# Performance work log

Measured on AMD Instinct MI355X. Metric: run time of the kernel, lower is better.

## Reference

```python
import jax, jax.numpy as jnp
import numpy as np

B, D = 2048, 1024
TEMP = 0.1
LAMBDA_CS_REG = 0.5


def setup_inputs() -> dict:
    key = jax.random.key(0)
    k1, k2, k3, k4, k5 = jax.random.split(key, 5)
    return {
        "english": jax.random.normal(k1, (B, D), dtype=jnp.float32),
        "etok": jax.random.normal(k2, (B, D), dtype=jnp.float32),
        "ktoe": jax.random.normal(k3, (B, D), dtype=jnp.float32),
        "korean": jax.random.normal(k4, (B, D), dtype=jnp.float32),
        "cs_ratios": jax.random.uniform(k5, (B,), dtype=jnp.float32),
    }


def _l2norm(x):
    return x / jnp.linalg.norm(x, axis=1, keepdims=True)


def reference(english, etok, ktoe, korean, cs_ratios):
    e = _l2norm(english)   # [B,D]
    et = _l2norm(etok)
    kt = _l2norm(ktoe)
    k = _l2norm(korean)
    bsz = e.shape[0]

    # Stack the 4 embedding types: order [english, korean, etok, ktoe]
    embs = jnp.stack([e, k, et, kt])           # [4,B,D]

    # Similarities of each anchor row i against every row j of every type t.
    S_e = jnp.einsum("bd,tnd->tbn", e, embs) / TEMP   # [4,B,B] english anchors
    S_k = jnp.einsum("bd,tnd->tbn", k, embs) / TEMP   # [4,B,B] korean anchors
    exp_Se = jnp.exp(S_e)
    exp_Sk = jnp.exp(S_k)

    diag_e = jnp.diagonal(exp_Se, axis1=1, axis2=2)   # [4,B] exp(sim(anchor_i, type_i))
    diag_k = jnp.diagonal(exp_Sk, axis1=1, axis2=2)

    # Negatives: all 4 types for every j != i.
    neg_e = exp_Se.sum(axis=(0, 2)) - diag_e.sum(axis=0)   # [B]
    neg_k = exp_Sk.sum(axis=(0, 2)) - diag_k.sum(axis=0)

    # Positives: eng anchor -> {etok_i, ktoe_i, korean_i}; kor anchor -> {etok_i, ktoe_i, english_i}
    num_e = diag_e[1] + diag_e[2] + diag_e[3]
    num_k = diag_k[0] + diag_k[2] + diag_k[3]

    loss_e = -jnp.log(num_e / (num_e + neg_e))
    loss_k = -jnp.log(num_k / (num_k + neg_k))
    contrastive_loss = (loss_e + loss_k).sum() / (2 * bsz)

    # Code-switch regularization
    r = cs_ratios[:, None]                              # [B,1]
    etok_reg = jnp.linalg.norm(et - (r * e + (1 - r) * k), axis=1)
    ktoe_reg = jnp.linalg.norm(kt - ((1 - r) * e + r * k), axis=1)
    cs_reg_loss = (etok_reg + ktoe_reg).sum() / bsz

    total_loss = contrastive_loss + LAMBDA_CS_REG * cs_reg_loss
    return total_loss, contrastive_loss, cs_reg_loss
```

## Files before the change

kernel.cpp:

```cpp
#include <hip/hip_runtime.h>
#include <math.h>

#define NB   2048
#define ND   1024
#define INV_TEMP 10.0f
#define LAMBDA_CS 0.5f

using short8  = __attribute__((ext_vector_type(8))) short;
using floatx4 = __attribute__((ext_vector_type(4))) float;

__device__ __forceinline__ ushort f32_to_bf16_rne(float f) {
  union { float f; unsigned u; } v; v.f = f;
  unsigned u = v.u;
  u += 0x7FFFu + ((u >> 16) & 1u);
  return (ushort)(u >> 16);
}

__global__ __launch_bounds__(256) void k_norm_reg(
    const float* __restrict__ e, const float* __restrict__ k,
    const float* __restrict__ et, const float* __restrict__ kt,
    const float* __restrict__ ratios,
    ushort* __restrict__ M, float* __restrict__ reg_partial,
    float* __restrict__ rowsum)
{
  const int b = blockIdx.x, tid = threadIdx.x;
  const int wave = tid >> 6, lane = tid & 63;

  float4 ve  = ((const float4*)(e  + (size_t)b * ND))[tid];
  float4 vk  = ((const float4*)(k  + (size_t)b * ND))[tid];
  float4 vet = ((const float4*)(et + (size_t)b * ND))[tid];
  float4 vkt = ((const float4*)(kt + (size_t)b * ND))[tid];

  float s0 = ve.x*ve.x + ve.y*ve.y + ve.z*ve.z + ve.w*ve.w;
  float s1 = vk.x*vk.x + vk.y*vk.y + vk.z*vk.z + vk.w*vk.w;
  float s2 = vet.x*vet.x + vet.y*vet.y + vet.z*vet.z + vet.w*vet.w;
  float s3 = vkt.x*vkt.x + vkt.y*vkt.y + vkt.z*vkt.z + vkt.w*vkt.w;
  #pragma unroll
  for (int o = 1; o < 64; o <<= 1) {
    s0 += __shfl_xor(s0, o); s1 += __shfl_xor(s1, o);
    s2 += __shfl_xor(s2, o); s3 += __shfl_xor(s3, o);
  }
  __shared__ float red[4][4];
  if (lane == 0) { red[wave][0] = s0; red[wave][1] = s1; red[wave][2] = s2; red[wave][3] = s3; }
  __syncthreads();
  const float ie  = 1.0f / sqrtf(red[0][0] + red[1][0] + red[2][0] + red[3][0]);
  const float ik  = 1.0f / sqrtf(red[0][1] + red[1][1] + red[2][1] + red[3][1]);
  const float iet = 1.0f / sqrtf(red[0][2] + red[1][2] + red[2][2] + red[3][2]);
  const float ikt = 1.0f / sqrtf(red[0][3] + red[1][3] + red[2][3] + red[3][3]);

  {
    ushort o4[4];
    o4[0] = f32_to_bf16_rne(ve.x * ie);  o4[1] = f32_to_bf16_rne(ve.y * ie);
    o4[2] = f32_to_bf16_rne(ve.z * ie);  o4[3] = f32_to_bf16_rne(ve.w * ie);
    *(ushort4*)(M + ((size_t)0 * NB + b) * ND + tid * 4) = *(ushort4*)o4;
    o4[0] = f32_to_bf16_rne(vk.x * ik);  o4[1] = f32_to_bf16_rne(vk.y * ik);
    o4[2] = f32_to_bf16_rne(vk.z * ik);  o4[3] = f32_to_bf16_rne(vk.w * ik);
    *(ushort4*)(M + ((size_t)1 * NB + b) * ND + tid * 4) = *(ushort4*)o4;
    o4[0] = f32_to_bf16_rne(vet.x * iet); o4[1] = f32_to_bf16_rne(vet.y * iet);
    o4[2] = f32_to_bf16_rne(vet.z * iet); o4[3] = f32_to_bf16_rne(vet.w * iet);
    *(ushort4*)(M + ((size_t)2 * NB + b) * ND + tid * 4) = *(ushort4*)o4;
    o4[0] = f32_to_bf16_rne(vkt.x * ikt); o4[1] = f32_to_bf16_rne(vkt.y * ikt);
    o4[2] = f32_to_bf16_rne(vkt.z * ikt); o4[3] = f32_to_bf16_rne(vkt.w * ikt);
    *(ushort4*)(M + ((size_t)3 * NB + b) * ND + tid * 4) = *(ushort4*)o4;
  }

  const float r = ratios[b], rm = 1.0f - r;
  float a1 = 0.f, a2 = 0.f;
  {
    float en, kn, d1, d2;
    en = ve.x*ie; kn = vk.x*ik;
    d1 = vet.x*iet - (r*en + rm*kn); d2 = vkt.x*ikt - (rm*en + r*kn);
    a1 += d1*d1; a2 += d2*d2;
    en = ve.y*ie; kn = vk.y*ik;
    d1 = vet.y*iet - (r*en + rm*kn); d2 = vkt.y*ikt - (rm*en + r*kn);
    a1 += d1*d1; a2 += d2*d2;
    en = ve.z*ie; kn = vk.z*ik;
    d1 = vet.z*iet - (r*en + rm*kn); d2 = vkt.z*ikt - (rm*en + r*kn);
    a1 += d1*d1; a2 += d2*d2;
    en = ve.w*ie; kn = vk.w*ik;
    d1 = vet.w*iet - (r*en + rm*kn); d2 = vkt.w*ikt - (rm*en + r*kn);
    a1 += d1*d1; a2 += d2*d2;
  }
  #pragma unroll
  for (int o = 1; o < 64; o <<= 1) { a1 += __shfl_xor(a1, o); a2 += __shfl_xor(a2, o); }
  __shared__ float red2[4][2];
  if (lane == 0) { red2[wave][0] = a1; red2[wave][1] = a2; }
  __syncthreads();
  if (tid == 0) {
    float t1 = red2[0][0] + red2[1][0] + red2[2][0] + red2[3][0];
    float t2 = red2[0][1] + red2[1][1] + red2[2][1] + red2[3][1];
    reg_partial[b] = sqrtf(t1) + sqrtf(t2);
    rowsum[b] = 0.f;
    rowsum[NB + b] = 0.f;
  }
}


#define GLDS(GP, LP)                                                           \
  __builtin_amdgcn_global_load_lds(                                            \
      (const __attribute__((address_space(1))) unsigned int*)(GP),             \
      (__attribute__((address_space(3))) unsigned int*)(LP), 16, 0, 0)

#define STAGE(TT, BUF) do {                                                    \
  GLDS(gA + (size_t)(c0 * 16 + srow) * ND + (TT) * 32 + scol * 8,              \
       &As[BUF][c0 * 512]);                                                    \
  GLDS(gA + (size_t)(c1 * 16 + srow) * ND + (TT) * 32 + scol * 8,              \
       &As[BUF][c1 * 512]);                                                    \
  GLDS(gB + (size_t)(c0 * 16 + srow) * ND + (TT) * 32 + scol * 8,              \
       &Bs[BUF][c0 * 512]);                                                    \
  GLDS(gB + (size_t)(c1 * 16 + srow) * ND + (TT) * 32 + scol * 8,              \
       &Bs[BUF][c1 * 512]);                                                    \
} while (0)

__global__ __launch_bounds__(256, 3) void k_gemm_exp_rowsum(
    const ushort* __restrict__ M,
    float* __restrict__ rowsum,
    float* __restrict__ diag)
{
  __shared__ __align__(16) ushort As[3][4096];
  __shared__ __align__(16) ushort Bs[3][4096];
  __shared__ float redR[256];
  __shared__ float redC[256];

  int bx, by;
  {
    int idx = blockIdx.x;
    if (idx < 1024) { by = idx >> 5; bx = 32 + (idx & 31); }
    else {
      int t = idx - 1024; by = 0;
      while (t >= 32 - by) { t -= 32 - by; ++by; }
      bx = by + t;
    }
  }
  const bool sym = (bx < 32) && (bx > by);
  const int j0 = bx * 128;
  const int i0 = by * 128;

  const int tid  = threadIdx.x;
  const int wave = tid >> 6;
  const int lane = tid & 63;
  const int q = lane >> 4;
  const int m = lane & 15;
  const int wrow = (wave >> 1) * 64;
  const int wcol = (wave & 1) * 64;

  floatx4 acc[4][4] = {};

  const int srow = lane >> 2;
  const int scol = (lane & 3) ^ ((srow >> 1) & 3);
  const int c0 = wave * 2, c1 = c0 + 1;

  const ushort* gA = M + (size_t)i0 * ND;
  const ushort* gB = M + (size_t)j0 * ND;

  int aoff[4], boff[4];
  #pragma unroll
  for (int x = 0; x < 4; ++x) {
    const int sw = (q ^ ((m >> 1) & 3)) * 8;
    aoff[x] = (wrow + x * 16 + m) * 32 + sw;
    boff[x] = (wcol + x * 16 + m) * 32 + sw;
  }

  STAGE(0, 0);
  STAGE(1, 1);
  asm volatile("s_waitcnt vmcnt(4)" ::: "memory");
  __builtin_amdgcn_s_barrier();

  int bcur = 0, bnext = 1, bstage = 2;
  #pragma unroll 1
  for (int t = 0; t < 32; ++t) {
    STAGE((t + 2) & 31, bstage);

    short8 af[4], bf[4];
    #pragma unroll
    for (int x = 0; x < 4; ++x) {
      af[x] = *(const short8*)&As[bcur][aoff[x]];
      bf[x] = *(const short8*)&Bs[bcur][boff[x]];
    }
    asm volatile("s_waitcnt lgkmcnt(0)" ::: "memory");
    __builtin_amdgcn_sched_barrier(0);

    __builtin_amdgcn_s_setprio(1);
    #pragma unroll
    for (int mi = 0; mi < 4; ++mi)
      #pragma unroll
      for (int ni = 0; ni < 4; ++ni)
        acc[mi][ni] = __builtin_amdgcn_mfma_f32_16x16x32_bf16(
            af[mi], bf[ni], acc[mi][ni], 0, 0, 0);
    __builtin_amdgcn_s_setprio(0);

    asm volatile("s_waitcnt vmcnt(4)" ::: "memory");
    __builtin_amdgcn_s_barrier();

    const int tmp = bcur; bcur = bnext; bnext = bstage; bstage = tmp;
  }

  __syncthreads();

  float colAcc[4] = {0.f, 0.f, 0.f, 0.f};
  #pragma unroll
  for (int mi = 0; mi < 4; ++mi) {
    #pragma unroll
    for (int r = 0; r < 4; ++r) {
      const int ig = i0 + wrow + mi * 16 + q * 4 + r;
      float s = 0.f;
      #pragma unroll
      for (int ni = 0; ni < 4; ++ni) {
        const float v = __expf(acc[mi][ni][r] * INV_TEMP);
        s += v;
        colAcc[ni] += v;
        const int jg = j0 + wcol + ni * 16 + m;
        if (((ig ^ jg) & (NB - 1)) == 0) {
          diag[(((ig >> 11) << 2) + (jg >> 11)) * NB + (ig & (NB - 1))] = v;
        }
      }
      s += __shfl_xor(s, 1);
      s += __shfl_xor(s, 2);
      s += __shfl_xor(s, 4);
      s += __shfl_xor(s, 8);
      if (m == 0) redR[(wave & 1) * 128 + wrow + mi * 16 + q * 4 + r] = s;
    }
  }
  #pragma unroll
  for (int ni = 0; ni < 4; ++ni) {
    float c = colAcc[ni];
    c += __shfl_xor(c, 16);
    c += __shfl_xor(c, 32);
    if (q == 0) redC[(wave >> 1) * 128 + wcol + ni * 16 + m] = c;
  }
  __syncthreads();
  if (tid < 128) {
    atomicAdd(&rowsum[i0 + tid], redR[tid] + redR[128 + tid]);
    if (sym)
      atomicAdd(&rowsum[j0 + tid], redC[tid] + redC[128 + tid]);
  }
}

__global__ __launch_bounds__(1024) void k_final(
    const float* __restrict__ rowsum, const float* __restrict__ diag,
    const float* __restrict__ reg_partial, float* __restrict__ out)
{
  const int tid = threadIdx.x;
  const int wave = tid >> 6, lane = tid & 63;
  float l = 0.f, g = 0.f;
  #pragma unroll
  for (int h = 0; h < 2; ++h) {
    const int n = tid + h * 1024;
    const float se = rowsum[n];
    const float sk = rowsum[NB + n];
    const float d_ee  = diag[0 * NB + n];
    const float d_ek  = diag[1 * NB + n];
    const float d_eet = diag[2 * NB + n];
    const float d_ekt = diag[3 * NB + n];
    const float d_kk  = diag[5 * NB + n];
    const float d_ket = diag[6 * NB + n];
    const float d_kkt = diag[7 * NB + n];
    const float num_e = d_ek + d_eet + d_ekt;
    const float num_k = d_ek + d_ket + d_kkt;
    l += logf((se - d_ee) / num_e) + logf((sk - d_kk) / num_k);
    g += reg_partial[n];
  }
  #pragma unroll
  for (int o = 1; o < 64; o <<= 1) { l += __shfl_xor(l, o); g += __shfl_xor(g, o); }
  __shared__ float rl[16], rg[16];
  if (lane == 0) { rl[wave] = l; rg[wave] = g; }
  __syncthreads();
  if (tid == 0) {
    float L = 0.f, G = 0.f;
    #pragma unroll
    for (int i = 0; i < 16; ++i) { L += rl[i]; G += rg[i]; }
    const float contrastive = L * (1.0f / (2.0f * NB));
    const float cs = G * (1.0f / NB);
    out[0] = contrastive + LAMBDA_CS * cs;
    out[1] = contrastive;
    out[2] = cs;
  }
}

extern "C" void kernel_launch(void* const* d_in, const int* in_sizes, int n_in,
                              void* d_out, int out_size, void* d_ws, size_t ws_size,
                              hipStream_t stream) {
  const float* english = (const float*)d_in[0];
  const float* etok    = (const float*)d_in[1];
  const float* ktoe    = (const float*)d_in[2];
  const float* korean  = (const float*)d_in[3];
  const float* ratios  = (const float*)d_in[4];

  char* ws = (char*)d_ws;
  const size_t OFF_M    = 0;
  const size_t OFF_ROW  = OFF_M + (size_t)8192 * 1024 * 2;
  const size_t OFF_DIAG = OFF_ROW + (size_t)4096 * 4;
  const size_t OFF_REG  = OFF_DIAG + 8 * NB * sizeof(float);

  ushort* M           = (ushort*)(ws + OFF_M);
  float* rowsum       = (float*)(ws + OFF_ROW);
  float* diag         = (float*)(ws + OFF_DIAG);
  float* reg_partial  = (float*)(ws + OFF_REG);

  k_norm_reg<<<dim3(NB), 256, 0, stream>>>(english, korean, etok, ktoe, ratios, M, reg_partial, rowsum);
  k_gemm_exp_rowsum<<<dim3(1552), 256, 0, stream>>>(M, rowsum, diag);
  k_final<<<dim3(1), 1024, 0, stream>>>(rowsum, diag, reg_partial, (float*)d_out);
}
```

Baseline: 168.1 us.

## Replace triple-buffered K=32 GEMM pipeline with single-buffered K=64 tiles

Drops the 3-stage global_load_lds prefetch pipeline (32-wide K slices, manual waitcnt and setprio) in favour of a single shared buffer holding 64-wide K slices. Each iteration loads with __syncthreads fences on both sides and then runs two MFMA sub-steps, using a new XOR swizzle over 8 columns. This halves the number of K iterations and barriers and simplifies the LDS layout. The cost is that global-load latency is no longer hidden behind MFMA work, and the launch bound no longer requests 3 blocks per CU.

```diff
diff --git a/kernel.cpp b/kernel.cpp
--- a/kernel.cpp
+++ b/kernel.cpp
@@ -101,24 +101,13 @@
       (const __attribute__((address_space(1))) unsigned int*)(GP),             \
       (__attribute__((address_space(3))) unsigned int*)(LP), 16, 0, 0)
 
-#define STAGE(TT, BUF) do {                                                    \
-  GLDS(gA + (size_t)(c0 * 16 + srow) * ND + (TT) * 32 + scol * 8,              \
-       &As[BUF][c0 * 512]);                                                    \
-  GLDS(gA + (size_t)(c1 * 16 + srow) * ND + (TT) * 32 + scol * 8,              \
-       &As[BUF][c1 * 512]);                                                    \
-  GLDS(gB + (size_t)(c0 * 16 + srow) * ND + (TT) * 32 + scol * 8,              \
-       &Bs[BUF][c0 * 512]);                                                    \
-  GLDS(gB + (size_t)(c1 * 16 + srow) * ND + (TT) * 32 + scol * 8,              \
-       &Bs[BUF][c1 * 512]);                                                    \
-} while (0)
-
-__global__ __launch_bounds__(256, 3) void k_gemm_exp_rowsum(
+__global__ __launch_bounds__(256) void k_gemm_exp_rowsum(
     const ushort* __restrict__ M,
     float* __restrict__ rowsum,
     float* __restrict__ diag)
 {
-  __shared__ __align__(16) ushort As[3][4096];
-  __shared__ __align__(16) ushort Bs[3][4096];
+  __shared__ __align__(16) ushort As[128 * 64];
+  __shared__ __align__(16) ushort Bs[128 * 64];
   __shared__ float redR[256];
   __shared__ float redC[256];
 
@@ -146,56 +135,46 @@
 
   floatx4 acc[4][4] = {};
 
-  const int srow = lane >> 2;
-  const int scol = (lane & 3) ^ ((srow >> 1) & 3);
-  const int c0 = wave * 2, c1 = c0 + 1;
-
+  const int sr8 = lane >> 3;
+  const int sc8 = (lane & 7) ^ (sr8 & 7);
   const ushort* gA = M + (size_t)i0 * ND;
   const ushort* gB = M + (size_t)j0 * ND;
 
   int aoff[4], boff[4];
   #pragma unroll
   for (int x = 0; x < 4; ++x) {
-    const int sw = (q ^ ((m >> 1) & 3)) * 8;
-    aoff[x] = (wrow + x * 16 + m) * 32 + sw;
-    boff[x] = (wcol + x * 16 + m) * 32 + sw;
-  }
-
-  STAGE(0, 0);
-  STAGE(1, 1);
-  asm volatile("s_waitcnt vmcnt(4)" ::: "memory");
-  __builtin_amdgcn_s_barrier();
-
-  int bcur = 0, bnext = 1, bstage = 2;
-  #pragma unroll 1
-  for (int t = 0; t < 32; ++t) {
-    STAGE((t + 2) & 31, bstage);
-
-    short8 af[4], bf[4];
-    #pragma unroll
-    for (int x = 0; x < 4; ++x) {
-      af[x] = *(const short8*)&As[bcur][aoff[x]];
-      bf[x] = *(const short8*)&Bs[bcur][boff[x]];
-    }
-    asm volatile("s_waitcnt lgkmcnt(0)" ::: "memory");
-    __builtin_amdgcn_sched_barrier(0);
-
-    __builtin_amdgcn_s_setprio(1);
-    #pragma unroll
-    for (int mi = 0; mi < 4; ++mi)
+    const int rA = wrow + x * 16 + m;
+    aoff[x] = rA * 64 + ((q * 8) ^ ((rA & 7) * 8));
+    const int rB = wcol + x * 16 + m;
+    boff[x] = rB * 64 + ((q * 8) ^ ((rB & 7) * 8));
+  }
+
+  for (int k0 = 0; k0 < ND; k0 += 64) {
+    __syncthreads();
+    #pragma unroll
+    for (int g = 0; g < 4; ++g) {
+      const int rbase = wave * 32 + g * 8;
+      GLDS(gA + (size_t)(rbase + sr8) * ND + k0 + sc8 * 8, &As[rbase * 64]);
+      GLDS(gB + (size_t)(rbase + sr8) * ND + k0 + sc8 * 8, &Bs[rbase * 64]);
+    }
+    __syncthreads();
+
+    #pragma unroll
+    for (int kk = 0; kk < 2; ++kk) {
+      short8 af[4], bf[4];
       #pragma unroll
-      for (int ni = 0; ni < 4; ++ni)
-        acc[mi][ni] = __builtin_amdgcn_mfma_f32_16x16x32_bf16(
-            af[mi], bf[ni], acc[mi][ni], 0, 0, 0);
-    __builtin_amdgcn_s_setprio(0);
-
-    asm volatile("s_waitcnt vmcnt(4)" ::: "memory");
-    __builtin_amdgcn_s_barrier();
-
-    const int tmp = bcur; bcur = bnext; bnext = bstage; bstage = tmp;
-  }
-
-  __syncthreads();
+      for (int x = 0; x < 4; ++x) {
+        af[x] = *(const short8*)&As[aoff[x] ^ (kk * 32)];
+        bf[x] = *(const short8*)&Bs[boff[x] ^ (kk * 32)];
+      }
+      #pragma unroll
+      for (int mi = 0; mi < 4; ++mi)
+        #pragma unroll
+        for (int ni = 0; ni < 4; ++ni)
+          acc[mi][ni] = __builtin_amdgcn_mfma_f32_16x16x32_bf16(
+              af[mi], bf[ni], acc[mi][ni], 0, 0, 0);
+    }
+  }
 
   float colAcc[4] = {0.f, 0.f, 0.f, 0.f};
   #pragma unroll
```

Result: slower. 171.8 us (+2.2%).

## Fuse final loss reduction into GEMM kernel via last-block atomic counter

Applied to the files above, without the earlier changes.

Removes the separate single-block final kernel and instead has the last finishing GEMM block (detected via an atomic counter reset in the norm kernel) compute the loss reduction. Diagonal stores become atomicExch so they are visible across blocks, and threadfences are added. Separately, the GEMM loop drops the explicit lgkmcnt wait, sched_barrier and setprio hints and relaxes the launch_bounds occupancy hint, leaving scheduling to the compiler. This saves one kernel launch but adds atomics/fences to every block and may change the main loop's codegen.

```diff
diff --git a/kernel.cpp b/kernel.cpp
--- a/kernel.cpp
+++ b/kernel.cpp
@@ -21,7 +21,7 @@
     const float* __restrict__ et, const float* __restrict__ kt,
     const float* __restrict__ ratios,
     ushort* __restrict__ M, float* __restrict__ reg_partial,
-    float* __restrict__ rowsum)
+    float* __restrict__ rowsum, int* __restrict__ counter)
 {
   const int b = blockIdx.x, tid = threadIdx.x;
   const int wave = tid >> 6, lane = tid & 63;
@@ -92,6 +92,7 @@
     reg_partial[b] = sqrtf(t1) + sqrtf(t2);
     rowsum[b] = 0.f;
     rowsum[NB + b] = 0.f;
+    if (b == 0) counter[0] = 0;
   }
 }
 
@@ -112,15 +113,19 @@
        &Bs[BUF][c1 * 512]);                                                    \
 } while (0)
 
-__global__ __launch_bounds__(256, 3) void k_gemm_exp_rowsum(
+__global__ __launch_bounds__(256) void k_gemm_exp_rowsum(
     const ushort* __restrict__ M,
     float* __restrict__ rowsum,
-    float* __restrict__ diag)
+    float* __restrict__ diag,
+    const float* __restrict__ reg_partial,
+    int* __restrict__ counter,
+    float* __restrict__ out)
 {
   __shared__ __align__(16) ushort As[3][4096];
   __shared__ __align__(16) ushort Bs[3][4096];
   __shared__ float redR[256];
   __shared__ float redC[256];
+  __shared__ int lastFlag;
 
   int bx, by;
   {
@@ -177,17 +182,12 @@
       af[x] = *(const short8*)&As[bcur][aoff[x]];
       bf[x] = *(const short8*)&Bs[bcur][boff[x]];
     }
-    asm volatile("s_waitcnt lgkmcnt(0)" ::: "memory");
-    __builtin_amdgcn_sched_barrier(0);
-
-    __builtin_amdgcn_s_setprio(1);
     #pragma unroll
     for (int mi = 0; mi < 4; ++mi)
       #pragma unroll
       for (int ni = 0; ni < 4; ++ni)
         acc[mi][ni] = __builtin_amdgcn_mfma_f32_16x16x32_bf16(
             af[mi], bf[ni], acc[mi][ni], 0, 0, 0);
-    __builtin_amdgcn_s_setprio(0);
 
     asm volatile("s_waitcnt vmcnt(4)" ::: "memory");
     __builtin_amdgcn_s_barrier();
@@ -211,7 +211,7 @@
         colAcc[ni] += v;
         const int jg = j0 + wcol + ni * 16 + m;
         if (((ig ^ jg) & (NB - 1)) == 0) {
-          diag[(((ig >> 11) << 2) + (jg >> 11)) * NB + (ig & (NB - 1))] = v;
+          atomicExch(&diag[(((ig >> 11) << 2) + (jg >> 11)) * NB + (ig & (NB - 1))], v);
         }
       }
       s += __shfl_xor(s, 1);
@@ -234,18 +234,20 @@
     if (sym)
       atomicAdd(&rowsum[j0 + tid], redC[tid] + redC[128 + tid]);
   }
-}
-
-__global__ __launch_bounds__(1024) void k_final(
-    const float* __restrict__ rowsum, const float* __restrict__ diag,
-    const float* __restrict__ reg_partial, float* __restrict__ out)
-{
-  const int tid = threadIdx.x;
-  const int wave = tid >> 6, lane = tid & 63;
+
+  __threadfence();
+  if (tid == 0) {
+    const int old = atomicAdd(counter, 1);
+    lastFlag = (old == (int)gridDim.x - 1);
+  }
+  __syncthreads();
+  if (!lastFlag) return;
+  __threadfence();
+
   float l = 0.f, g = 0.f;
   #pragma unroll
-  for (int h = 0; h < 2; ++h) {
-    const int n = tid + h * 1024;
+  for (int i = 0; i < 8; ++i) {
+    const int n = tid + i * 256;
     const float se = rowsum[n];
     const float sk = rowsum[NB + n];
     const float d_ee  = diag[0 * NB + n];
@@ -262,13 +264,11 @@
   }
   #pragma unroll
   for (int o = 1; o < 64; o <<= 1) { l += __shfl_xor(l, o); g += __shfl_xor(g, o); }
-  __shared__ float rl[16], rg[16];
-  if (lane == 0) { rl[wave] = l; rg[wave] = g; }
+  if (lane == 0) { redR[wave] = l; redR[8 + wave] = g; }
   __syncthreads();
   if (tid == 0) {
-    float L = 0.f, G = 0.f;
-    #pragma unroll
-    for (int i = 0; i < 16; ++i) { L += rl[i]; G += rg[i]; }
+    const float L = redR[0] + redR[1] + redR[2] + redR[3];
+    const float G = redR[8] + redR[9] + redR[10] + redR[11];
     const float contrastive = L * (1.0f / (2.0f * NB));
     const float cs = G * (1.0f / NB);
     out[0] = contrastive + LAMBDA_CS * cs;
@@ -291,13 +291,17 @@
   const size_t OFF_ROW  = OFF_M + (size_t)8192 * 1024 * 2;
   const size_t OFF_DIAG = OFF_ROW + (size_t)4096 * 4;
   const size_t OFF_REG  = OFF_DIAG + 8 * NB * sizeof(float);
+  const size_t OFF_CNT  = OFF_REG + NB * sizeof(float);
 
   ushort* M           = (ushort*)(ws + OFF_M);
   float* rowsum       = (float*)(ws + OFF_ROW);
   float* diag         = (float*)(ws + OFF_DIAG);
   float* reg_partial  = (float*)(ws + OFF_REG);
-
-  k_norm_reg<<<dim3(NB), 256, 0, stream>>>(english, korean, etok, ktoe, ratios, M, reg_partial, rowsum);
-  k_gemm_exp_rowsum<<<dim3(1552), 256, 0, stream>>>(M, rowsum, diag);
-  k_final<<<dim3(1), 1024, 0, stream>>>(rowsum, diag, reg_partial, (float*)d_out);
+  int*   counter      = (int*)(ws + OFF_CNT);
+
+  k_norm_reg<<<dim3(NB), 256, 0, stream>>>(english, korean, etok, ktoe, ratios,
+                                           M, reg_partial, rowsum, counter);
+  k_gemm_exp_rowsum<<<dim3(1552), 256, 0, stream>>>(M, rowsum, diag,
+                                                    reg_partial, counter,
+                                                    (float*)d_out);
 }
```

Measured after the change: 269.0 us. 1.6x slower.

## Replace triple-buffered LDS pipeline with double buffering and full barriers

Applied to the files above, without the earlier changes.

The GEMM main loop moves from a 3-stage LDS ring with manual vmcnt waits, sched barriers and setprio to a 2-stage ping-pong. Each stage is bounded by __syncthreads and the loop is unrolled by two. This cuts LDS use per block and drops the occupancy hint from the launch bounds, which could allow more resident blocks and simplifies the schedule. In exchange, prefetch depth falls to one tile and each barrier waits for all outstanding loads, so global load latency is less hidden.

```diff
diff --git a/kernel.cpp b/kernel.cpp
--- a/kernel.cpp
+++ b/kernel.cpp
@@ -112,13 +112,28 @@
        &Bs[BUF][c1 * 512]);                                                    \
 } while (0)
 
-__global__ __launch_bounds__(256, 3) void k_gemm_exp_rowsum(
+#define COMPUTE(BUF) do {                                                      \
+  short8 af_[4], bf_[4];                                                       \
+  _Pragma("unroll")                                                            \
+  for (int x = 0; x < 4; ++x) {                                                \
+    af_[x] = *(const short8*)&As[BUF][aoff[x]];                                \
+    bf_[x] = *(const short8*)&Bs[BUF][boff[x]];                                \
+  }                                                                            \
+  _Pragma("unroll")                                                            \
+  for (int mi_ = 0; mi_ < 4; ++mi_)                                            \
+    _Pragma("unroll")                                                          \
+    for (int ni_ = 0; ni_ < 4; ++ni_)                                          \
+      acc[mi_][ni_] = __builtin_amdgcn_mfma_f32_16x16x32_bf16(                 \
+          af_[mi_], bf_[ni_], acc[mi_][ni_], 0, 0, 0);                         \
+} while (0)
+
+__global__ __launch_bounds__(256) void k_gemm_exp_rowsum(
     const ushort* __restrict__ M,
     float* __restrict__ rowsum,
     float* __restrict__ diag)
 {
-  __shared__ __align__(16) ushort As[3][4096];
-  __shared__ __align__(16) ushort Bs[3][4096];
+  __shared__ __align__(16) ushort As[2][4096];
+  __shared__ __align__(16) ushort Bs[2][4096];
   __shared__ float redR[256];
   __shared__ float redC[256];
 
@@ -162,40 +177,15 @@
   }
 
   STAGE(0, 0);
-  STAGE(1, 1);
-  asm volatile("s_waitcnt vmcnt(4)" ::: "memory");
-  __builtin_amdgcn_s_barrier();
-
-  int bcur = 0, bnext = 1, bstage = 2;
   #pragma unroll 1
-  for (int t = 0; t < 32; ++t) {
-    STAGE((t + 2) & 31, bstage);
-
-    short8 af[4], bf[4];
-    #pragma unroll
-    for (int x = 0; x < 4; ++x) {
-      af[x] = *(const short8*)&As[bcur][aoff[x]];
-      bf[x] = *(const short8*)&Bs[bcur][boff[x]];
-    }
-    asm volatile("s_waitcnt lgkmcnt(0)" ::: "memory");
-    __builtin_amdgcn_sched_barrier(0);
-
-    __builtin_amdgcn_s_setprio(1);
-    #pragma unroll
-    for (int mi = 0; mi < 4; ++mi)
-      #pragma unroll
-      for (int ni = 0; ni < 4; ++ni)
-        acc[mi][ni] = __builtin_amdgcn_mfma_f32_16x16x32_bf16(
-            af[mi], bf[ni], acc[mi][ni], 0, 0, 0);
-    __builtin_amdgcn_s_setprio(0);
-
-    asm volatile("s_waitcnt vmcnt(4)" ::: "memory");
-    __builtin_amdgcn_s_barrier();
-
-    const int tmp = bcur; bcur = bnext; bnext = bstage; bstage = tmp;
-  }
-
-  __syncthreads();
+  for (int t = 0; t < 32; t += 2) {
+    __syncthreads();
+    STAGE(t + 1, 1);
+    COMPUTE(0);
+    __syncthreads();
+    if (t + 2 < 32) STAGE(t + 2, 0);
+    COMPUTE(1);
+  }
 
   float colAcc[4] = {0.f, 0.f, 0.f, 0.f};
   #pragma unroll
@@ -297,7 +287,8 @@
   float* diag         = (float*)(ws + OFF_DIAG);
   float* reg_partial  = (float*)(ws + OFF_REG);
 
-  k_norm_reg<<<dim3(NB), 256, 0, stream>>>(english, korean, etok, ktoe, ratios, M, reg_partial, rowsum);
+  k_norm_reg<<<dim3(NB), 256, 0, stream>>>(english, korean, etok, ktoe, ratios,
+                                           M, reg_partial, rowsum);
   k_gemm_exp_rowsum<<<dim3(1552), 256, 0, stream>>>(M, rowsum, diag);
   k_final<<<dim3(1), 1024, 0, stream>>>(rowsum, diag, reg_partial, (float*)d_out);
 }
```

Result: no change. 170.8 us (+1.6%).
